# Kernel tuning notes

Measured on AMD Instinct MI355X. Metric: run time of the kernel, lower is better.

## Reference

```python
import jax, jax.numpy as jnp
import numpy as np

D_MODEL = 1024
N_HEADS = 16
HEAD_DIM = D_MODEL // N_HEADS


def setup_inputs() -> dict:
    key = jax.random.key(0)
    ks = jax.random.split(key, 5)
    B, S = 4, 2048
    scale = 1.0 / np.sqrt(D_MODEL)
    return {
        "x": jax.random.normal(ks[0], (B, S, D_MODEL), dtype=jnp.float32),
        "W_q": jax.random.normal(ks[1], (D_MODEL, D_MODEL), dtype=jnp.float32) * scale,
        "W_k": jax.random.normal(ks[2], (D_MODEL, D_MODEL), dtype=jnp.float32) * scale,
        "W_v": jax.random.normal(ks[3], (D_MODEL, D_MODEL), dtype=jnp.float32) * scale,
        "W_o": jax.random.normal(ks[4], (D_MODEL, D_MODEL), dtype=jnp.float32) * scale,
    }


def reference(x, W_q, W_k, W_v, W_o):
    B, S, _ = x.shape
    # nn.Linear(d,d,bias=False): y = x @ W.T ; W stored as (out,in)
    def proj(W):
        y = jnp.einsum('bsd,ed->bse', x, W)
        return y.reshape(B, S, N_HEADS, HEAD_DIM).transpose(0, 2, 1, 3)  # (B,H,S,Dh)
    q, k, v = proj(W_q), proj(W_k), proj(W_v)
    scores = jnp.einsum('bhqd,bhkd->bhqk', q, k) / np.sqrt(HEAD_DIM)
    causal = jnp.tril(jnp.ones((S, S), dtype=bool))  # (S,S)
    scores = jnp.where(causal[None, None], scores, -jnp.inf)
    attn = jax.nn.softmax(scores, axis=-1)
    heads = jnp.einsum('bhqk,bhkd->bhqd', attn, v)
    concat = heads.transpose(0, 2, 1, 3).reshape(B, S, D_MODEL)
    return jnp.einsum('bsd,ed->bse', concat, W_o)
```

## Files before the change

### kernel.cpp

```cpp
#include <hip/hip_runtime.h>
#include <hip/hip_bf16.h>

#define D_MODEL 1024
#define N_HEADS 16
#define HEAD_DIM 64
#define BATCH 4
#define SEQ 2048
#define M_ROWS (BATCH * SEQ)

typedef __attribute__((ext_vector_type(8))) __bf16 bf16x8;
typedef __attribute__((ext_vector_type(8))) short short8;
typedef __attribute__((ext_vector_type(4))) float f32x4;

static __device__ __forceinline__ unsigned short f2bf_rne(float f) {
  unsigned int u = __float_as_uint(f);
  u += 0x7FFFu + ((u >> 16) & 1u);
  return (unsigned short)(u >> 16);
}

#if __has_builtin(__builtin_amdgcn_exp2f)
#define EXP2F(x) __builtin_amdgcn_exp2f(x)
#else
#define EXP2F(x) exp2f(x)
#endif

static __device__ __forceinline__ void gl_lds16(const unsigned short* g, unsigned short* l) {
  __builtin_amdgcn_global_load_lds((const __attribute__((address_space(1))) unsigned int*)g,
                                   (__attribute__((address_space(3))) unsigned int*)l, 16, 0, 0);
}

__global__ __launch_bounds__(256) void cvt_all(const float* __restrict__ x,
                                               const float* __restrict__ wq,
                                               const float* __restrict__ wk,
                                               const float* __restrict__ wv,
                                               const float* __restrict__ wo,
                                               unsigned short* __restrict__ xb,
                                               unsigned short* __restrict__ wqb,
                                               unsigned short* __restrict__ wkb,
                                               unsigned short* __restrict__ wvb,
                                               unsigned short* __restrict__ wob) {
  const int bid = blockIdx.x;
  const float* src;
  unsigned short* dst;
  int i;
  if (bid < 8192) {
    src = x; dst = xb; i = bid * 256 + threadIdx.x;
  } else {
    int r = bid - 8192;
    int w = r >> 10;
    i = (r & 1023) * 256 + threadIdx.x;
    switch (w) {
      case 0: src = wq; dst = wqb; break;
      case 1: src = wk; dst = wkb; break;
      case 2: src = wv; dst = wvb; break;
      default: src = wo; dst = wob; break;
    }
  }
  float4 f = reinterpret_cast<const float4*>(src)[i];
  ushort4 o;
  o.x = f2bf_rne(f.x); o.y = f2bf_rne(f.y); o.z = f2bf_rne(f.z); o.w = f2bf_rne(f.w);
  reinterpret_cast<ushort4*>(dst)[i] = o;
}

__global__ __launch_bounds__(256) void qkv_gemm(const unsigned short* __restrict__ A,
                                                const unsigned short* __restrict__ Wq,
                                                const unsigned short* __restrict__ Wk,
                                                const unsigned short* __restrict__ Wv,
                                                unsigned short* __restrict__ Qo,
                                                unsigned short* __restrict__ Ko,
                                                unsigned short* __restrict__ Vt) {
  __shared__ __align__(16) unsigned short smem[16384];
  const int t = threadIdx.x;
  const int widx = blockIdx.x >> 3;
  const int bn = blockIdx.x & 7, bm = blockIdx.y;
  const unsigned short* Bw = (widx == 0) ? Wq : (widx == 1) ? Wk : Wv;
  const float oscale = (widx == 0) ? 0.18033688f : 1.0f;
  const int K = D_MODEL, N = D_MODEL;

  const int wave = t >> 6, lane = t & 63;
  const int wm = (wave >> 1) * 64, wn = (wave & 1) * 64;
  const int lr = lane & 15, quad = lane >> 4;

  const int g0 = wave * 128 + lane, g1 = g0 + 64;
  const int r0 = g0 >> 2, c0 = (g0 & 3) << 3;
  const int r1 = g1 >> 2, c1 = (g1 & 3) << 3;
  const unsigned short* Arow0 = A + (size_t)(bm * 128 + r0) * K + c0;
  const unsigned short* Arow1 = A + (size_t)(bm * 128 + r1) * K + c1;
  const unsigned short* Brow0 = Bw + (size_t)(bn * 128 + r0) * K + c0;
  const unsigned short* Brow1 = Bw + (size_t)(bn * 128 + r1) * K + c1;

  f32x4 acc[4][4] = {};

  gl_lds16(Arow0, &smem[g0 * 8]);
  gl_lds16(Arow1, &smem[g1 * 8]);
  gl_lds16(Brow0, &smem[4096 + g0 * 8]);
  gl_lds16(Brow1, &smem[4096 + g1 * 8]);
  __syncthreads();

  for (int it = 0; it < 32; it++) {
    const int cur = (it & 1) * 8192;
    if (it + 1 < 32) {
      const int nxt = 8192 - cur;
      const int k1 = (it + 1) * 32;
      gl_lds16(Arow0 + k1, &smem[nxt + g0 * 8]);
      gl_lds16(Arow1 + k1, &smem[nxt + g1 * 8]);
      gl_lds16(Brow0 + k1, &smem[nxt + 4096 + g0 * 8]);
      gl_lds16(Brow1 + k1, &smem[nxt + 4096 + g1 * 8]);
    }
    const unsigned short* As = &smem[cur];
    const unsigned short* Bs = &smem[cur + 4096];

    bf16x8 af[4], bfr[4];
#pragma unroll
    for (int mt = 0; mt < 4; mt++)
      af[mt] = __builtin_bit_cast(
          bf16x8, *reinterpret_cast<const short8*>(&As[(wm + mt * 16 + lr) * 32 + quad * 8]));
#pragma unroll
    for (int nt = 0; nt < 4; nt++)
      bfr[nt] = __builtin_bit_cast(
          bf16x8, *reinterpret_cast<const short8*>(&Bs[(wn + nt * 16 + lr) * 32 + quad * 8]));
#pragma unroll
    for (int mt = 0; mt < 4; mt++)
#pragma unroll
      for (int nt = 0; nt < 4; nt++)
        acc[mt][nt] = __builtin_amdgcn_mfma_f32_16x16x32_bf16(af[mt], bfr[nt], acc[mt][nt], 0, 0, 0);
    __syncthreads();
  }

  if (widx < 2) {
    unsigned short* Cp = (widx == 0) ? Qo : Ko;
#pragma unroll
    for (int mt = 0; mt < 4; mt++) {
#pragma unroll
      for (int nt = 0; nt < 4; nt++) {
        int col = bn * 128 + wn + nt * 16 + lr;
#pragma unroll
        for (int r = 0; r < 4; r++) {
          int row = bm * 128 + wm + mt * 16 + quad * 4 + r;
          Cp[(size_t)row * N + col] = f2bf_rne(acc[mt][nt][r] * oscale);
        }
      }
    }
  } else {
    const int b = bm >> 4;
    const int s0 = (bm & 15) * 128;
#pragma unroll
    for (int half = 0; half < 2; half++) {
      __syncthreads();
      if ((wave & 1) == half) {
#pragma unroll
        for (int nt = 0; nt < 4; nt++) {
#pragma unroll
          for (int mt = 0; mt < 4; mt++) {
#pragma unroll
            for (int r = 0; r < 4; r++) {
              int cl = nt * 16 + lr;
              int rl = wm + mt * 16 + quad * 4 + r;
              smem[cl * 136 + rl] = f2bf_rne(acc[mt][nt][r]);
            }
          }
        }
      }
      __syncthreads();
      const int h2 = bn * 2 + half;
      const size_t rowbase = ((size_t)(b * N_HEADS + h2)) * HEAD_DIM;
#pragma unroll
      for (int i = 0; i < 4; i++) {
        int c = i * 256 + t;
        int d = c >> 4, s8 = (c & 15) * 8;
        uint4 v = *reinterpret_cast<const uint4*>(&smem[d * 136 + s8]);
        *reinterpret_cast<uint4*>(Vt + (rowbase + d) * SEQ + s0 + s8) = v;
      }
    }
  }
}

__global__ __launch_bounds__(256) void gemm_bt_f32(const unsigned short* __restrict__ A,
                                                   const unsigned short* __restrict__ Bw,
                                                   float* __restrict__ Cp,
                                                   int M, int N, int K) {
  __shared__ __align__(16) unsigned short smem[16384];
  const int t = threadIdx.x;
  const int bn = blockIdx.x, bm = blockIdx.y;
  const int wave = t >> 6, lane = t & 63;
  const int wm = (wave >> 1) * 64, wn = (wave & 1) * 64;
  const int lr = lane & 15, quad = lane >> 4;

  const int g0 = wave * 128 + lane, g1 = g0 + 64;
  const int r0 = g0 >> 2, c0 = (g0 & 3) << 3;
  const int r1 = g1 >> 2, c1 = (g1 & 3) << 3;
  const unsigned short* Arow0 = A + (size_t)(bm * 128 + r0) * K + c0;
  const unsigned short* Arow1 = A + (size_t)(bm * 128 + r1) * K + c1;
  const unsigned short* Brow0 = Bw + (size_t)(bn * 128 + r0) * K + c0;
  const unsigned short* Brow1 = Bw + (size_t)(bn * 128 + r1) * K + c1;

  f32x4 acc[4][4] = {};

  gl_lds16(Arow0, &smem[g0 * 8]);
  gl_lds16(Arow1, &smem[g1 * 8]);
  gl_lds16(Brow0, &smem[4096 + g0 * 8]);
  gl_lds16(Brow1, &smem[4096 + g1 * 8]);
  __syncthreads();

  const int niter = K / 32;
  for (int it = 0; it < niter; it++) {
    const int cur = (it & 1) * 8192;
    if (it + 1 < niter) {
      const int nxt = 8192 - cur;
      const int k1 = (it + 1) * 32;
      gl_lds16(Arow0 + k1, &smem[nxt + g0 * 8]);
      gl_lds16(Arow1 + k1, &smem[nxt + g1 * 8]);
      gl_lds16(Brow0 + k1, &smem[nxt + 4096 + g0 * 8]);
      gl_lds16(Brow1 + k1, &smem[nxt + 4096 + g1 * 8]);
    }
    const unsigned short* As = &smem[cur];
    const unsigned short* Bs = &smem[cur + 4096];

    bf16x8 af[4], bfr[4];
#pragma unroll
    for (int mt = 0; mt < 4; mt++)
      af[mt] = __builtin_bit_cast(
          bf16x8, *reinterpret_cast<const short8*>(&As[(wm + mt * 16 + lr) * 32 + quad * 8]));
#pragma unroll
    for (int nt = 0; nt < 4; nt++)
      bfr[nt] = __builtin_bit_cast(
          bf16x8, *reinterpret_cast<const short8*>(&Bs[(wn + nt * 16 + lr) * 32 + quad * 8]));
#pragma unroll
    for (int mt = 0; mt < 4; mt++)
#pragma unroll
      for (int nt = 0; nt < 4; nt++)
        acc[mt][nt] = __builtin_amdgcn_mfma_f32_16x16x32_bf16(af[mt], bfr[nt], acc[mt][nt], 0, 0, 0);
    __syncthreads();
  }

#pragma unroll
  for (int mt = 0; mt < 4; mt++) {
#pragma unroll
    for (int nt = 0; nt < 4; nt++) {
      int col = bn * 128 + wn + nt * 16 + lr;
#pragma unroll
      for (int r = 0; r < 4; r++) {
        int row = bm * 128 + wm + mt * 16 + quad * 4 + r;
        Cp[(size_t)row * N + col] = acc[mt][nt][r];
      }
    }
  }
}

__global__ __launch_bounds__(256, 4) void attn_causal(const unsigned short* __restrict__ Q,
                                                      const unsigned short* __restrict__ Km,
                                                      const unsigned short* __restrict__ Vt,
                                                      unsigned short* __restrict__ O) {
  __shared__ __align__(16) unsigned short Ks[64 * 72];
  __shared__ __align__(16) unsigned short Vs[64 * 72];
  __shared__ __align__(16) unsigned short Ps[4][16 * 72];

  const int bid = blockIdx.x;
  const int p = bid & 15;
  const int h = (bid >> 4) & 15;
  const int b = bid >> 8;

  const int t = threadIdx.x;
  const int wave = t >> 6, lane = t & 63;
  const int lr = lane & 15, quad = lane >> 4;

  const size_t base = (size_t)b * SEQ * D_MODEL + h * HEAD_DIM;
  const unsigned short* Qb = Q + base;
  const unsigned short* Kb = Km + base;
  const unsigned short* Vb = Vt + (size_t)(b * N_HEADS + h) * HEAD_DIM * SEQ;
  unsigned short* pw = &Ps[wave][0];

  const int sr = t >> 3, sc = (t & 7) << 3;

  for (int ph = 0; ph < 2; ph++) {
    const int qt = ph ? (31 - p) : p;
    const int m0 = qt * 64 + wave * 16;
    const int ntiles = qt + 1;

    bf16x8 qf[2];
#pragma unroll
    for (int kk = 0; kk < 2; kk++)
      qf[kk] = __builtin_bit_cast(
          bf16x8,
          *reinterpret_cast<const short8*>(Qb + (size_t)(m0 + lr) * D_MODEL + kk * 32 + quad * 8));

    f32x4 o_acc[4] = {};
    float lsum[4] = {};

    uint4 ra = *reinterpret_cast<const uint4*>(Kb + (size_t)sr * D_MODEL + sc);
    uint4 rb = *reinterpret_cast<const uint4*>(Kb + (size_t)(sr + 32) * D_MODEL + sc);
    uint4 rc = *reinterpret_cast<const uint4*>(Vb + (size_t)sr * SEQ + sc);
    uint4 rd = *reinterpret_cast<const uint4*>(Vb + (size_t)(sr + 32) * SEQ + sc);

    for (int kt = 0; kt < ntiles; kt++) {
      const int kv0 = kt * 64;
      __syncthreads();
      *reinterpret_cast<uint4*>(&Ks[sr * 72 + sc]) = ra;
      *reinterpret_cast<uint4*>(&Ks[(sr + 32) * 72 + sc]) = rb;
      *reinterpret_cast<uint4*>(&Vs[sr * 72 + sc]) = rc;
      *reinterpret_cast<uint4*>(&Vs[(sr + 32) * 72 + sc]) = rd;
      __syncthreads();
      if (kt + 1 < ntiles) {
        const int kv1 = kv0 + 64;
        ra = *reinterpret_cast<const uint4*>(Kb + (size_t)(kv1 + sr) * D_MODEL + sc);
        rb = *reinterpret_cast<const uint4*>(Kb + (size_t)(kv1 + sr + 32) * D_MODEL + sc);
        rc = *reinterpret_cast<const uint4*>(Vb + (size_t)sr * SEQ + kv1 + sc);
        rd = *reinterpret_cast<const uint4*>(Vb + (size_t)(sr + 32) * SEQ + kv1 + sc);
      }

      f32x4 sAcc[4] = {};
#pragma unroll
      for (int kk = 0; kk < 2; kk++) {
        bf16x8 kf[4];
#pragma unroll
        for (int j = 0; j < 4; j++)
          kf[j] = __builtin_bit_cast(
              bf16x8, *reinterpret_cast<const short8*>(&Ks[(j * 16 + lr) * 72 + kk * 32 + quad * 8]));
#pragma unroll
        for (int j = 0; j < 4; j++)
          sAcc[j] = __builtin_amdgcn_mfma_f32_16x16x32_bf16(qf[kk], kf[j], sAcc[j], 0, 0, 0);
      }

      asm volatile("s_waitcnt lgkmcnt(0)" ::: "memory");
#pragma unroll
      for (int r = 0; r < 4; r++) {
        const int qpos = m0 + quad * 4 + r;
        float e[4];
#pragma unroll
        for (int j = 0; j < 4; j++) e[j] = EXP2F(sAcc[j][r]);
        if (kt == ntiles - 1) {
#pragma unroll
          for (int j = 0; j < 4; j++)
            if (kv0 + j * 16 + lr > qpos) e[j] = 0.f;
        }
        lsum[r] += (e[0] + e[1]) + (e[2] + e[3]);
        unsigned short* pr = &pw[(quad * 4 + r) * 72];
#pragma unroll
        for (int j = 0; j < 4; j++) pr[j * 16 + lr] = f2bf_rne(e[j]);
      }
      asm volatile("s_waitcnt lgkmcnt(0)" ::: "memory");

#pragma unroll
      for (int kk = 0; kk < 2; kk++) {
        bf16x8 pf = __builtin_bit_cast(
            bf16x8, *reinterpret_cast<const short8*>(&pw[lr * 72 + kk * 32 + quad * 8]));
#pragma unroll
        for (int c = 0; c < 4; c++) {
          bf16x8 vv = __builtin_bit_cast(
              bf16x8, *reinterpret_cast<const short8*>(&Vs[(c * 16 + lr) * 72 + kk * 32 + quad * 8]));
          o_acc[c] = __builtin_amdgcn_mfma_f32_16x16x32_bf16(pf, vv, o_acc[c], 0, 0, 0);
        }
      }
    }

#pragma unroll
    for (int r = 0; r < 4; r++) {
      float l = lsum[r];
#pragma unroll
      for (int off = 1; off < 16; off <<= 1) l += __shfl_xor(l, off, 64);
      const float inv = 1.f / l;
      const int qpos = m0 + quad * 4 + r;
#pragma unroll
      for (int c = 0; c < 4; c++)
        O[base + (size_t)qpos * D_MODEL + c * 16 + lr] = f2bf_rne(o_acc[c][r] * inv);
    }
  }
}

extern "C" void kernel_launch(void* const* d_in, const int* in_sizes, int n_in,
                              void* d_out, int out_size, void* d_ws, size_t ws_size,
                              hipStream_t stream) {
  const float* x  = (const float*)d_in[0];
  const float* Wq = (const float*)d_in[1];
  const float* Wk = (const float*)d_in[2];
  const float* Wv = (const float*)d_in[3];
  const float* Wo = (const float*)d_in[4];
  float* out = (float*)d_out;

  char* ws = (char*)d_ws;
  const size_t SZ_X = (size_t)M_ROWS * D_MODEL * 2;
  const size_t SZ_W = (size_t)D_MODEL * D_MODEL * 2;
  unsigned short* xb  = (unsigned short*)(ws);
  unsigned short* wqb = (unsigned short*)(ws + SZ_X);
  unsigned short* wkb = (unsigned short*)(ws + SZ_X + 1 * SZ_W);
  unsigned short* wvb = (unsigned short*)(ws + SZ_X + 2 * SZ_W);
  unsigned short* wob = (unsigned short*)(ws + SZ_X + 3 * SZ_W);
  unsigned short* Qb  = (unsigned short*)(ws + 1 * SZ_X + 4 * SZ_W);
  unsigned short* Kb  = (unsigned short*)(ws + 2 * SZ_X + 4 * SZ_W);
  unsigned short* Vt  = (unsigned short*)(ws + 3 * SZ_X + 4 * SZ_W);
  unsigned short* Ob  = xb;

  cvt_all<<<12288, 256, 0, stream>>>(x, Wq, Wk, Wv, Wo, xb, wqb, wkb, wvb, wob);

  qkv_gemm<<<dim3(24, 64), 256, 0, stream>>>(xb, wqb, wkb, wvb, Qb, Kb, Vt);

  attn_causal<<<1024, 256, 0, stream>>>(Qb, Kb, Vt, Ob);

  gemm_bt_f32<<<dim3(8, 64), 256, 0, stream>>>(Ob, wob, out, M_ROWS, D_MODEL, D_MODEL);
}
```

Baseline: 276.5 us.

## Use 128-row query tiles in attention and narrower N tiles in output GEMM

The attention kernel now runs 512-thread blocks (8 waves) that each own 128 query rows, so every K/V tile staged in shared memory serves twice as many queries. Each thread now loads one K row and one V row per tile, and causal masking is applied to any tile that overlaps the diagonal. The output-projection GEMM switches from 128x128 to 128x64 tiles, doubling its grid to 1024 blocks for better CU occupancy at the cost of reloading A tiles more often. Risks: 512-thread blocks with launch_bounds(512,4) may limit registers, and the load balance of the paired causal tiles changes.

```diff
diff --git a/kernel.cpp b/kernel.cpp
--- a/kernel.cpp
+++ b/kernel.cpp
@@ -179,56 +179,54 @@
                                                    const unsigned short* __restrict__ Bw,
                                                    float* __restrict__ Cp,
                                                    int M, int N, int K) {
-  __shared__ __align__(16) unsigned short smem[16384];
+  __shared__ __align__(16) unsigned short smem[12288];
   const int t = threadIdx.x;
   const int bn = blockIdx.x, bm = blockIdx.y;
   const int wave = t >> 6, lane = t & 63;
-  const int wm = (wave >> 1) * 64, wn = (wave & 1) * 64;
+  const int wm = (wave >> 1) * 64, wn = (wave & 1) * 32;
   const int lr = lane & 15, quad = lane >> 4;
 
-  const int g0 = wave * 128 + lane, g1 = g0 + 64;
-  const int r0 = g0 >> 2, c0 = (g0 & 3) << 3;
-  const int r1 = g1 >> 2, c1 = (g1 & 3) << 3;
-  const unsigned short* Arow0 = A + (size_t)(bm * 128 + r0) * K + c0;
-  const unsigned short* Arow1 = A + (size_t)(bm * 128 + r1) * K + c1;
-  const unsigned short* Brow0 = Bw + (size_t)(bn * 128 + r0) * K + c0;
-  const unsigned short* Brow1 = Bw + (size_t)(bn * 128 + r1) * K + c1;
-
-  f32x4 acc[4][4] = {};
+  const int g0 = t, g1 = t + 256;
+  const int ar0 = g0 >> 2, ac0 = (g0 & 3) << 3;
+  const int ar1 = g1 >> 2, ac1 = (g1 & 3) << 3;
+  const int br = t >> 2, bc = (t & 3) << 3;
+  const unsigned short* Arow0 = A + (size_t)(bm * 128 + ar0) * K + ac0;
+  const unsigned short* Arow1 = A + (size_t)(bm * 128 + ar1) * K + ac1;
+  const unsigned short* Brow = Bw + (size_t)(bn * 64 + br) * K + bc;
+
+  f32x4 acc[4][2] = {};
 
   gl_lds16(Arow0, &smem[g0 * 8]);
   gl_lds16(Arow1, &smem[g1 * 8]);
-  gl_lds16(Brow0, &smem[4096 + g0 * 8]);
-  gl_lds16(Brow1, &smem[4096 + g1 * 8]);
+  gl_lds16(Brow, &smem[4096 + t * 8]);
   __syncthreads();
 
   const int niter = K / 32;
   for (int it = 0; it < niter; it++) {
-    const int cur = (it & 1) * 8192;
+    const int cur = (it & 1) * 6144;
     if (it + 1 < niter) {
-      const int nxt = 8192 - cur;
+      const int nxt = 6144 - cur;
       const int k1 = (it + 1) * 32;
       gl_lds16(Arow0 + k1, &smem[nxt + g0 * 8]);
       gl_lds16(Arow1 + k1, &smem[nxt + g1 * 8]);
-      gl_lds16(Brow0 + k1, &smem[nxt + 4096 + g0 * 8]);
-      gl_lds16(Brow1 + k1, &smem[nxt + 4096 + g1 * 8]);
+      gl_lds16(Brow + k1, &smem[nxt + 4096 + t * 8]);
     }
     const unsigned short* As = &smem[cur];
     const unsigned short* Bs = &smem[cur + 4096];
 
-    bf16x8 af[4], bfr[4];
+    bf16x8 af[4], bfr[2];
 #pragma unroll
     for (int mt = 0; mt < 4; mt++)
       af[mt] = __builtin_bit_cast(
           bf16x8, *reinterpret_cast<const short8*>(&As[(wm + mt * 16 + lr) * 32 + quad * 8]));
 #pragma unroll
-    for (int nt = 0; nt < 4; nt++)
+    for (int nt = 0; nt < 2; nt++)
       bfr[nt] = __builtin_bit_cast(
           bf16x8, *reinterpret_cast<const short8*>(&Bs[(wn + nt * 16 + lr) * 32 + quad * 8]));
 #pragma unroll
     for (int mt = 0; mt < 4; mt++)
 #pragma unroll
-      for (int nt = 0; nt < 4; nt++)
+      for (int nt = 0; nt < 2; nt++)
         acc[mt][nt] = __builtin_amdgcn_mfma_f32_16x16x32_bf16(af[mt], bfr[nt], acc[mt][nt], 0, 0, 0);
     __syncthreads();
   }
@@ -236,8 +234,8 @@
 #pragma unroll
   for (int mt = 0; mt < 4; mt++) {
 #pragma unroll
-    for (int nt = 0; nt < 4; nt++) {
-      int col = bn * 128 + wn + nt * 16 + lr;
+    for (int nt = 0; nt < 2; nt++) {
+      int col = bn * 64 + wn + nt * 16 + lr;
 #pragma unroll
       for (int r = 0; r < 4; r++) {
         int row = bm * 128 + wm + mt * 16 + quad * 4 + r;
@@ -247,18 +245,18 @@
   }
 }
 
-__global__ __launch_bounds__(256, 4) void attn_causal(const unsigned short* __restrict__ Q,
+__global__ __launch_bounds__(512, 4) void attn_causal(const unsigned short* __restrict__ Q,
                                                       const unsigned short* __restrict__ Km,
                                                       const unsigned short* __restrict__ Vt,
                                                       unsigned short* __restrict__ O) {
   __shared__ __align__(16) unsigned short Ks[64 * 72];
   __shared__ __align__(16) unsigned short Vs[64 * 72];
-  __shared__ __align__(16) unsigned short Ps[4][16 * 72];
+  __shared__ __align__(16) unsigned short Ps[8][16 * 72];
 
   const int bid = blockIdx.x;
-  const int p = bid & 15;
-  const int h = (bid >> 4) & 15;
-  const int b = bid >> 8;
+  const int p = bid & 7;
+  const int h = (bid >> 3) & 15;
+  const int b = bid >> 7;
 
   const int t = threadIdx.x;
   const int wave = t >> 6, lane = t & 63;
@@ -273,9 +271,9 @@
   const int sr = t >> 3, sc = (t & 7) << 3;
 
   for (int ph = 0; ph < 2; ph++) {
-    const int qt = ph ? (31 - p) : p;
-    const int m0 = qt * 64 + wave * 16;
-    const int ntiles = qt + 1;
+    const int qt = ph ? (15 - p) : p;
+    const int m0 = qt * 128 + wave * 16;
+    const int ntiles = (qt + 1) * 2;
 
     bf16x8 qf[2];
 #pragma unroll
@@ -288,24 +286,18 @@
     float lsum[4] = {};
 
     uint4 ra = *reinterpret_cast<const uint4*>(Kb + (size_t)sr * D_MODEL + sc);
-    uint4 rb = *reinterpret_cast<const uint4*>(Kb + (size_t)(sr + 32) * D_MODEL + sc);
     uint4 rc = *reinterpret_cast<const uint4*>(Vb + (size_t)sr * SEQ + sc);
-    uint4 rd = *reinterpret_cast<const uint4*>(Vb + (size_t)(sr + 32) * SEQ + sc);
 
     for (int kt = 0; kt < ntiles; kt++) {
       const int kv0 = kt * 64;
       __syncthreads();
       *reinterpret_cast<uint4*>(&Ks[sr * 72 + sc]) = ra;
-      *reinterpret_cast<uint4*>(&Ks[(sr + 32) * 72 + sc]) = rb;
       *reinterpret_cast<uint4*>(&Vs[sr * 72 + sc]) = rc;
-      *reinterpret_cast<uint4*>(&Vs[(sr + 32) * 72 + sc]) = rd;
       __syncthreads();
       if (kt + 1 < ntiles) {
         const int kv1 = kv0 + 64;
         ra = *reinterpret_cast<const uint4*>(Kb + (size_t)(kv1 + sr) * D_MODEL + sc);
-        rb = *reinterpret_cast<const uint4*>(Kb + (size_t)(kv1 + sr + 32) * D_MODEL + sc);
         rc = *reinterpret_cast<const uint4*>(Vb + (size_t)sr * SEQ + kv1 + sc);
-        rd = *reinterpret_cast<const uint4*>(Vb + (size_t)(sr + 32) * SEQ + kv1 + sc);
       }
 
       f32x4 sAcc[4] = {};
@@ -322,13 +314,14 @@
       }
 
       asm volatile("s_waitcnt lgkmcnt(0)" ::: "memory");
+      const bool needmask = (kv0 + 63 > m0);
 #pragma unroll
       for (int r = 0; r < 4; r++) {
         const int qpos = m0 + quad * 4 + r;
         float e[4];
 #pragma unroll
         for (int j = 0; j < 4; j++) e[j] = EXP2F(sAcc[j][r]);
-        if (kt == ntiles - 1) {
+        if (needmask) {
 #pragma unroll
           for (int j = 0; j < 4; j++)
             if (kv0 + j * 16 + lr > qpos) e[j] = 0.f;
@@ -394,7 +387,7 @@
 
   qkv_gemm<<<dim3(24, 64), 256, 0, stream>>>(xb, wqb, wkb, wvb, Qb, Kb, Vt);
 
-  attn_causal<<<1024, 256, 0, stream>>>(Qb, Kb, Vt, Ob);
-
-  gemm_bt_f32<<<dim3(8, 64), 256, 0, stream>>>(Ob, wob, out, M_ROWS, D_MODEL, D_MODEL);
-}
+  attn_causal<<<512, 512, 0, stream>>>(Qb, Kb, Vt, Ob);
+
+  gemm_bt_f32<<<dim3(16, 64), 256, 0, stream>>>(Ob, wob, out, M_ROWS, D_MODEL, D_MODEL);
+}
```

Measured after the change: 265.4 us. 1.04x faster.
